# Kernel tuning notes

Hardware: AMD Instinct MI355X
Metric: run time of the kernel (lower is better)

Reference implementation:

```python
import jax, jax.numpy as jnp
import numpy as np

B, L, D, H = 4, 2048, 512, 512


def setup_inputs() -> dict:
    key = jax.random.key(0)
    ks = jax.random.split(key, 7)
    scale = D ** (-0.5)
    return {
        "x": jax.random.normal(ks[0], (B, L, D), jnp.float32),
        "hidden": jax.random.normal(ks[1], (B, D, H), jnp.float32),
        "log_base_lr": jnp.asarray(np.log(0.01), jnp.float32),
        "log_base_weight_decay": jnp.asarray(np.log(0.99), jnp.float32),
        "Wq": jax.random.normal(ks[2], (H, D), jnp.float32) * scale,
        "Wk": jax.random.normal(ks[3], (H, D), jnp.float32) * scale,
        "Wv": jax.random.normal(ks[4], (D, D), jnp.float32) * scale,
        "fc_lr_w": jax.random.normal(ks[5], (1, D), jnp.float32) * scale,
        "fc_lr_b": jnp.zeros((1,), jnp.float32),
        "fc_wd_w": jax.random.normal(ks[6], (1, D), jnp.float32) * scale,
        "fc_wd_b": jnp.zeros((1,), jnp.float32),
    }


def reference(x, hidden, log_base_lr, log_base_weight_decay, Wq, Wk, Wv,
              fc_lr_w, fc_lr_b, fc_wd_w, fc_wd_b):
    b, l, d = x.shape
    W_prev = hidden                                      # (b, d, h)
    query = jnp.einsum('bld,hd->blh', x, Wq)             # (b, l, h)
    key = jnp.einsum('bld,hd->blh', x, Wk)               # (b, l, h)
    value = jnp.einsum('bld,ed->ble', x, Wv)             # (b, l, d)

    lr = jnp.exp(log_base_lr) * jax.nn.sigmoid(
        jnp.einsum('bld,d->bl', x, fc_lr_w[0]) + fc_lr_b[0])        # (b, l)
    log_weight_decay = jnp.log(
        jnp.exp(log_base_weight_decay) * jax.nn.sigmoid(
            jnp.einsum('bld,d->bl', x, fc_wd_w[0]) + fc_wd_b[0]))   # (b, l)

    # cross-chunk decay: exp of prefix-sum of log decays
    wd_cross = jnp.exp(jnp.cumsum(log_weight_decay, axis=1))        # (b, l)

    # inner-chunk decay mask: (b, m, l), strictly-upper cumsum then upper triu
    rep = jnp.broadcast_to(log_weight_decay[:, None, :], (b, l, l))
    wd_inner = jnp.triu(jnp.exp(jnp.cumsum(jnp.triu(rep, 1), axis=2)))

    kq = jnp.einsum('blh,bmh->blm', key, query)          # (b, l, m)
    mask_kq = kq * wd_inner                              # (b, l, m)

    WpK_V = jnp.einsum('bdh,blh->bld', W_prev, key) - value         # (b, l, d)

    y_inner = -jnp.einsum('bld,bl,blm->bld', WpK_V, lr, mask_kq)
    y_cross = jnp.einsum('bdh,blh,bl->bld', W_prev, key, wd_cross)
    y = y_inner + y_cross

    W_next_inner = -jnp.einsum('bld,bl,blh->bdh', WpK_V, lr * wd_inner[:, :, -1], key)
    W_next_cross = W_prev * wd_cross[:, -1][:, None, None]
    W_next = W_next_inner + W_next_cross
    return (y, W_next)
```

## Files before the change

kernel.cpp:

```cpp
#include <hip/hip_runtime.h>
#include <cstdint>
#include <cstddef>

#define B_ 4
#define L_ 2048
#define D_ 512
#define H_ 512
#define CH 64
#define NC (L_ / CH)
#define NS 4

typedef unsigned short u16;
typedef __attribute__((ext_vector_type(8))) short short8v;
typedef __attribute__((ext_vector_type(4))) float f32x4;

typedef __attribute__((address_space(3))) unsigned lds_uint;
typedef const __attribute__((address_space(1))) unsigned glob_uint;

__device__ __forceinline__ void glds16(const u16* g, const u16* l) {
    __builtin_amdgcn_global_load_lds((glob_uint*)g, (lds_uint*)l, 16, 0, 0);
}

__device__ __forceinline__ u16 bf16_rne(float x) {
    union { float f; unsigned u; } v; v.f = x;
    unsigned r = v.u + 0x7fffu + ((v.u >> 16) & 1u);
    return (u16)(r >> 16);
}
__device__ __forceinline__ float bf16_tof(u16 h) {
    union { unsigned u; float f; } v; v.u = ((unsigned)h) << 16;
    return v.f;
}

__global__ __launch_bounds__(256) void k_prep(
    const float* __restrict__ x, const float* __restrict__ flr_w, const float* __restrict__ flr_b,
    const float* __restrict__ fwd_w, const float* __restrict__ fwd_b,
    const float* __restrict__ lblr, const float* __restrict__ lbwd,
    float* __restrict__ lr, float* __restrict__ lwd, float* __restrict__ wd,
    u16* __restrict__ xh)
{
    int bx = blockIdx.x;
    int wave = threadIdx.x >> 6;
    int lane = threadIdx.x & 63;
    int row  = bx * 4 + wave;
    const float4* xr = (const float4*)(x + (size_t)row * D_);
    const float4* wl = (const float4*)flr_w;
    const float4* ww = (const float4*)fwd_w;
    float zl = 0.f, zw = 0.f;
#pragma unroll
    for (int i = 0; i < 2; ++i) {
        int idx = lane + i * 64;
        float4 xv = xr[idx];
        float4 av = wl[idx];
        float4 bv = ww[idx];
        zl += xv.x*av.x + xv.y*av.y + xv.z*av.z + xv.w*av.w;
        zw += xv.x*bv.x + xv.y*bv.y + xv.z*bv.z + xv.w*bv.w;
        ushort4 h4;
        h4.x = bf16_rne(xv.x); h4.y = bf16_rne(xv.y);
        h4.z = bf16_rne(xv.z); h4.w = bf16_rne(xv.w);
        *(ushort4*)(xh + (size_t)row * D_ + idx * 4) = h4;
    }
#pragma unroll
    for (int off = 32; off; off >>= 1) {
        zl += __shfl_xor(zl, off, 64);
        zw += __shfl_xor(zw, off, 64);
    }
    if (lane == 0) {
        zl += flr_b[0];
        zw += fwd_b[0];
        float lrv = expf(lblr[0]) / (1.f + expf(-zl));
        float ls = (zw >= 0.f) ? (-log1pf(expf(-zw))) : (zw - log1pf(expf(zw)));
        float lw = lbwd[0] + ls;
        lr[row]  = lrv;
        lwd[row] = lw;
        wd[row]  = expf(lw);
    }
}

__global__ __launch_bounds__(256) void k_cumsum(
    const float* __restrict__ lwd, const float* __restrict__ lr,
    const float* __restrict__ Wq, const float* __restrict__ Wk, const float* __restrict__ Wv,
    const float* __restrict__ hid,
    u16* __restrict__ Wqh, u16* __restrict__ Wkh, u16* __restrict__ Wvh, u16* __restrict__ Wph,
    float* __restrict__ cum, float* __restrict__ wdc, float* __restrict__ c)
{
    int bx = blockIdx.x;
    if (bx >= B_) {
        int idx = bx - B_;
        int y = idx >> 8;
        const size_t DH = (size_t)D_ * H_;
        const float* s; u16* d;
        if      (y == 0) { s = Wq; d = Wqh; }
        else if (y == 1) { s = Wk; d = Wkh; }
        else if (y == 2) { s = Wv; d = Wvh; }
        else             { s = hid + (size_t)(y - 3) * DH; d = Wph + (size_t)(y - 3) * DH; }
        int i = ((idx & 255) * 256 + threadIdx.x) * 4;
        float4 v = *(const float4*)(s + i);
        ushort4 h4;
        h4.x = bf16_rne(v.x); h4.y = bf16_rne(v.y);
        h4.z = bf16_rne(v.z); h4.w = bf16_rne(v.w);
        *(ushort4*)(d + i) = h4;
        return;
    }
    int b = bx;
    int t = threadIdx.x;
    const float* in = lwd + (size_t)b * L_;
    float v[8];
    float s = 0.f;
#pragma unroll
    for (int j = 0; j < 8; ++j) { s += in[t*8 + j]; v[j] = s; }
    __shared__ float sd[256];
    __shared__ float totb;
    sd[t] = s;
    __syncthreads();
    for (int d = 1; d < 256; d <<= 1) {
        float xv = (t >= d) ? sd[t - d] : 0.f;
        __syncthreads();
        sd[t] += xv;
        __syncthreads();
    }
    float excl = sd[t] - s;
    if (t == 255) totb = sd[255];
    __syncthreads();
    float total = totb;
#pragma unroll
    for (int j = 0; j < 8; ++j) {
        int l = t*8 + j;
        float cv = excl + v[j];
        cum[(size_t)b*L_ + l] = cv;
        wdc[(size_t)b*L_ + l] = expf(cv);
        c[(size_t)b*L_ + l]   = lr[(size_t)b*L_ + l] * expf(total - cv);
    }
}


__device__ __forceinline__ void tile_src(int base_row, int ld, size_t& g0, size_t& g1) {
    int tid = threadIdx.x;
    int r = tid >> 2;
    int sw = ((tid & 3) ^ ((r >> 1) & 3)) * 8;
    g0 = (size_t)(base_row + r) * ld + sw;
    g1 = g0 + (size_t)64 * ld;
}
__device__ __forceinline__ int frag_off(int wbase, int f) {
    int lane = threadIdx.x & 63;
    int ra = wbase + f * 16 + (lane & 15);
    return ra * 64 + (((lane >> 4) ^ ((ra >> 1) & 3)) * 16);
}
__device__ __forceinline__ void mfma44(f32x4 acc[4][4], const short8v a[4], const short8v b[4]) {
#pragma unroll
    for (int i = 0; i < 4; ++i)
#pragma unroll
        for (int j = 0; j < 4; ++j)
            acc[i][j] = __builtin_amdgcn_mfma_f32_16x16x32_bf16(a[i], b[j], acc[i][j], 0, 0, 0);
}

__device__ __forceinline__ void core_dualB(
    char* smem, const u16* __restrict__ A_g,
    const u16* __restrict__ B0_g, const u16* __restrict__ B1_g,
    int lda, int ldb, int K, int m0, int n0, f32x4 acc0[4][4], f32x4 acc1[4][4])
{
    const int wv = threadIdx.x >> 6;
    const int wm = wv >> 1, wn = wv & 1;
    size_t aLo, aHi, bLo, bHi;
    tile_src(m0, lda, aLo, aHi);
    tile_src(n0, ldb, bLo, bHi);
    const int dLo = wv * 1024, dHi = 4096 + wv * 1024;
    int offA[4], offB[4];
#pragma unroll
    for (int f = 0; f < 4; ++f) { offA[f] = frag_off(wm * 64, f); offB[f] = frag_off(wn * 64, f); }
    auto stage = [&](int bi, int k0) {
        glds16(A_g  + aLo + k0, (const u16*)(smem + bi * 8192 + dLo));
        glds16(A_g  + aHi + k0, (const u16*)(smem + bi * 8192 + dHi));
        glds16(B0_g + bLo + k0, (const u16*)(smem + 24576 + bi * 8192 + dLo));
        glds16(B0_g + bHi + k0, (const u16*)(smem + 24576 + bi * 8192 + dHi));
        glds16(B1_g + bLo + k0, (const u16*)(smem + 49152 + bi * 8192 + dLo));
        glds16(B1_g + bHi + k0, (const u16*)(smem + 49152 + bi * 8192 + dHi));
    };
    const int nt = K >> 5;
    stage(0, 0);
    stage(1, 32);
    int bi = 0, bs = 2;
    for (int t = 0; t < nt; ++t) {
        if (t + 1 < nt) asm volatile("s_waitcnt vmcnt(6)" ::: "memory");
        else            asm volatile("s_waitcnt vmcnt(0)" ::: "memory");
        __builtin_amdgcn_s_barrier();
        asm volatile("" ::: "memory");
        if (t + 2 < nt) stage(bs, (t + 2) << 5);
        const char* bA  = smem + bi * 8192;
        const char* bB0 = smem + 24576 + bi * 8192;
        const char* bB1 = smem + 49152 + bi * 8192;
        short8v a[4], p[4], q[4];
#pragma unroll
        for (int f = 0; f < 4; ++f) {
            a[f] = *(const short8v*)(bA  + offA[f]);
            p[f] = *(const short8v*)(bB0 + offB[f]);
            q[f] = *(const short8v*)(bB1 + offB[f]);
        }
        __builtin_amdgcn_s_setprio(1);
        mfma44(acc0, a, p);
        mfma44(acc1, a, q);
        __builtin_amdgcn_s_setprio(0);
        asm volatile("" ::: "memory");
        bi = (bi == 2) ? 0 : bi + 1;
        bs = (bs == 2) ? 0 : bs + 1;
    }
    asm volatile("" ::: "memory");
    __builtin_amdgcn_s_barrier();
}

__device__ __forceinline__ void core_dualAB(
    char* smem, const u16* __restrict__ A0_g, const u16* __restrict__ A1_g,
    const u16* __restrict__ B0_g, const u16* __restrict__ B1_g,
    int lda, int ldb, int K, int m0, int n0, f32x4 acc0[4][4], f32x4 acc1[4][4])
{
    const int wv = threadIdx.x >> 6;
    const int wm = wv >> 1, wn = wv & 1;
    size_t aLo, aHi, bLo, bHi;
    tile_src(m0, lda, aLo, aHi);
    tile_src(n0, ldb, bLo, bHi);
    const int dLo = wv * 1024, dHi = 4096 + wv * 1024;
    int offA[4], offB[4];
#pragma unroll
    for (int f = 0; f < 4; ++f) { offA[f] = frag_off(wm * 64, f); offB[f] = frag_off(wn * 64, f); }
    auto stage = [&](int bi, int k0) {
        glds16(A0_g + aLo + k0, (const u16*)(smem + bi * 8192 + dLo));
        glds16(A0_g + aHi + k0, (const u16*)(smem + bi * 8192 + dHi));
        glds16(A1_g + aLo + k0, (const u16*)(smem + 24576 + bi * 8192 + dLo));
        glds16(A1_g + aHi + k0, (const u16*)(smem + 24576 + bi * 8192 + dHi));
        glds16(B0_g + bLo + k0, (const u16*)(smem + 49152 + bi * 8192 + dLo));
        glds16(B0_g + bHi + k0, (const u16*)(smem + 49152 + bi * 8192 + dHi));
        glds16(B1_g + bLo + k0, (const u16*)(smem + 73728 + bi * 8192 + dLo));
        glds16(B1_g + bHi + k0, (const u16*)(smem + 73728 + bi * 8192 + dHi));
    };
    const int nt = K >> 5;
    stage(0, 0);
    stage(1, 32);
    int bi = 0, bs = 2;
    for (int t = 0; t < nt; ++t) {
        if (t + 1 < nt) asm volatile("s_waitcnt vmcnt(8)" ::: "memory");
        else            asm volatile("s_waitcnt vmcnt(0)" ::: "memory");
        __builtin_amdgcn_s_barrier();
        asm volatile("" ::: "memory");
        if (t + 2 < nt) stage(bs, (t + 2) << 5);
        const char* bA0 = smem + bi * 8192;
        const char* bA1 = smem + 24576 + bi * 8192;
        const char* bB0 = smem + 49152 + bi * 8192;
        const char* bB1 = smem + 73728 + bi * 8192;
        short8v a[4], c[4], p[4], q[4];
#pragma unroll
        for (int f = 0; f < 4; ++f) {
            a[f] = *(const short8v*)(bA0 + offA[f]);
            c[f] = *(const short8v*)(bA1 + offA[f]);
            p[f] = *(const short8v*)(bB0 + offB[f]);
            q[f] = *(const short8v*)(bB1 + offB[f]);
        }
        __builtin_amdgcn_s_setprio(1);
        mfma44(acc0, a, p);
        mfma44(acc1, c, q);
        __builtin_amdgcn_s_setprio(0);
        asm volatile("" ::: "memory");
        bi = (bi == 2) ? 0 : bi + 1;
        bs = (bs == 2) ? 0 : bs + 1;
    }
    asm volatile("" ::: "memory");
    __builtin_amdgcn_s_barrier();
}

__device__ __forceinline__ void core_single(
    char* smem, const u16* __restrict__ A_g, const u16* __restrict__ B_g,
    int lda, int ldb, int K, int m0, int n0, f32x4 acc[4][4])
{
    const int wv = threadIdx.x >> 6;
    const int wm = wv >> 1, wn = wv & 1;
    size_t aLo, aHi, bLo, bHi;
    tile_src(m0, lda, aLo, aHi);
    tile_src(n0, ldb, bLo, bHi);
    const int dLo = wv * 1024, dHi = 4096 + wv * 1024;
    int offA[4], offB[4];
#pragma unroll
    for (int f = 0; f < 4; ++f) { offA[f] = frag_off(wm * 64, f); offB[f] = frag_off(wn * 64, f); }
    auto stage = [&](int bi, int k0) {
        glds16(A_g + aLo + k0, (const u16*)(smem + bi * 8192 + dLo));
        glds16(A_g + aHi + k0, (const u16*)(smem + bi * 8192 + dHi));
        glds16(B_g + bLo + k0, (const u16*)(smem + 24576 + bi * 8192 + dLo));
        glds16(B_g + bHi + k0, (const u16*)(smem + 24576 + bi * 8192 + dHi));
    };
    const int nt = K >> 5;
    stage(0, 0);
    stage(1, 32);
    int bi = 0, bs = 2;
    for (int t = 0; t < nt; ++t) {
        if (t + 1 < nt) asm volatile("s_waitcnt vmcnt(4)" ::: "memory");
        else            asm volatile("s_waitcnt vmcnt(0)" ::: "memory");
        __builtin_amdgcn_s_barrier();
        asm volatile("" ::: "memory");
        if (t + 2 < nt) stage(bs, (t + 2) << 5);
        const char* bA = smem + bi * 8192;
        const char* bB = smem + 24576 + bi * 8192;
        short8v a[4], p[4];
#pragma unroll
        for (int f = 0; f < 4; ++f) {
            a[f] = *(const short8v*)(bA + offA[f]);
            p[f] = *(const short8v*)(bB + offB[f]);
        }
        __builtin_amdgcn_s_setprio(1);
        mfma44(acc, a, p);
        __builtin_amdgcn_s_setprio(0);
        asm volatile("" ::: "memory");
        bi = (bi == 2) ? 0 : bi + 1;
        bs = (bs == 2) ? 0 : bs + 1;
    }
    asm volatile("" ::: "memory");
    __builtin_amdgcn_s_barrier();
}

__global__ __launch_bounds__(256, 1) void k_mfma_qk(
    const u16* __restrict__ xh,
    const u16* __restrict__ Wqh, const u16* __restrict__ Wkh,
    const float* __restrict__ cvec, const float* __restrict__ wd,
    u16* __restrict__ kh, u16* __restrict__ kcth, u16* __restrict__ Gloc)
{
    __shared__ __align__(16) char smem[73728];
    __shared__ float pwd[128];
    int flat = blockIdx.x;
    flat = (flat & 7) * 32 + (flat >> 3);
    int n0 = (flat & 3) * 128;
    int m0 = (flat >> 2) * 128;
    f32x4 accq[4][4], acck[4][4];
#pragma unroll
    for (int i = 0; i < 4; ++i)
#pragma unroll
    for (int j = 0; j < 4; ++j) { accq[i][j] = 0.f; acck[i][j] = 0.f; }
    core_dualB(smem, xh, Wqh, Wkh, D_, D_, D_, m0, n0, accq, acck);

    const int lane = threadIdx.x & 63;
    const int wv = threadIdx.x >> 6, wm = wv >> 1, wn = wv & 1;
    const int colq = lane & 15, rq = lane >> 4;

#pragma unroll
    for (int mf = 0; mf < 4; ++mf) {
        int grow0 = m0 + wm*64 + mf*16 + rq*4;
        float cv[4];
#pragma unroll
        for (int r = 0; r < 4; ++r) cv[r] = cvec[grow0 + r];
#pragma unroll
        for (int nf = 0; nf < 4; ++nf) {
            int gc = n0 + wn*64 + nf*16 + colq;
            f32x4 a = acck[mf][nf];
            ushort4 hc;
#pragma unroll
            for (int r = 0; r < 4; ++r) {
                kh[(size_t)(grow0 + r) * H_ + gc] = bf16_rne(a[r]);
                ((u16*)&hc)[r] = bf16_rne(cv[r] * a[r]);
            }
            int b = grow0 >> 11, lloc = grow0 & 2047;
            size_t tbase = (size_t)b * (H_ * L_) + (size_t)gc * L_ + lloc;
            *(ushort4*)(kcth + tbase) = hc;
        }
    }

    u16* g = (u16*)smem;
#pragma unroll
    for (int mf = 0; mf < 4; ++mf) {
        int rl0 = wm*64 + mf*16 + rq*4;
#pragma unroll
        for (int nf = 0; nf < 4; ++nf) {
            int cl = wn*64 + nf*16 + colq;
#pragma unroll
            for (int r = 0; r < 4; ++r)
                g[(rl0 + r)*128 + cl] = bf16_rne(accq[mf][nf][r]);
        }
    }
    if (threadIdx.x < 128) pwd[threadIdx.x] = wd[m0 + threadIdx.x];
    __syncthreads();
    {
        int col = threadIdx.x & 127;
        int base = (threadIdx.x >> 7) * 64;
        float G = bf16_tof(g[(base + 63)*128 + col]);
        for (int l = 62; l >= 0; --l) {
            float qv = bf16_tof(g[(base + l)*128 + col]);
            G = fmaf(pwd[base + l + 1], G, qv);
            g[(base + l)*128 + col] = bf16_rne(G);
        }
    }
    __syncthreads();
    int row = threadIdx.x >> 1, c0 = (threadIdx.x & 1) * 64;
    u16* dst = Gloc + (size_t)(m0 + row) * H_ + n0 + c0;
#pragma unroll
    for (int j = 0; j < 8; ++j)
        *(int4*)(dst + j*8) = *(const int4*)&g[row*128 + c0 + j*8];
}

__global__ __launch_bounds__(64) void k_scan_carry(
    const float* __restrict__ cum, const u16* __restrict__ Gloc, float* __restrict__ Gs)
{
    int b = blockIdx.x;
    int h = blockIdx.y * 64 + threadIdx.x;
    __shared__ float dec[NC];
    const float* cb = cum + (size_t)b * L_;
    if (threadIdx.x < NC - 1) dec[threadIdx.x] = expf(cb[(threadIdx.x + 1) * CH] - cb[threadIdx.x * CH]);
    __syncthreads();
    const u16* g = Gloc + (size_t)b * L_ * H_ + h;
    float* gs = Gs + (size_t)b * NC * H_ + h;
    float v[NC];
#pragma unroll
    for (int c = 0; c < NC; ++c)
        v[c] = bf16_tof(g[(size_t)(c * CH) * H_]);
    float G = v[NC - 1];
    gs[(size_t)(NC - 1) * H_] = G;
#pragma unroll
    for (int c = NC - 2; c >= 0; --c) {
        G = fmaf(dec[c], G, v[c]);
        gs[(size_t)c * H_] = G;
    }
}

__global__ __launch_bounds__(256) void k_sdot(
    const u16* __restrict__ kh,
    const u16* __restrict__ Gloc, const float* __restrict__ Gs,
    const float* __restrict__ cum, float* __restrict__ S)
{
    int wave = threadIdx.x >> 6, lane = threadIdx.x & 63;
    int row = blockIdx.x * 4 + wave;
    int b = row >> 11, l = row & 2047;
    int c = l / CH;
    float a = 0.f;
    const float* gsr = Gs;
    if (c < NC - 1) {
        a = expf(cum[((size_t)b << 11) + (size_t)((c + 1) * CH)] - cum[row]);
        gsr = Gs + ((size_t)(b * NC + c + 1)) * H_;
    }
    const u16* khr = kh + (size_t)row * H_;
    const u16* glr = Gloc + (size_t)row * H_;
    const float4* gq = (const float4*)gsr;
    float s = 0.f;
    int base = lane * 8;
    ushort4 h0 = *(const ushort4*)(khr + base);
    ushort4 h1 = *(const ushort4*)(khr + base + 4);
    ushort4 g0 = *(const ushort4*)(glr + base);
    ushort4 g1 = *(const ushort4*)(glr + base + 4);
    float4 s0 = gq[lane * 2];
    float4 s1 = gq[lane * 2 + 1];
    s += bf16_tof(h0.x) * fmaf(a, s0.x, bf16_tof(g0.x));
    s += bf16_tof(h0.y) * fmaf(a, s0.y, bf16_tof(g0.y));
    s += bf16_tof(h0.z) * fmaf(a, s0.z, bf16_tof(g0.z));
    s += bf16_tof(h0.w) * fmaf(a, s0.w, bf16_tof(g0.w));
    s += bf16_tof(h1.x) * fmaf(a, s1.x, bf16_tof(g1.x));
    s += bf16_tof(h1.y) * fmaf(a, s1.y, bf16_tof(g1.y));
    s += bf16_tof(h1.z) * fmaf(a, s1.z, bf16_tof(g1.z));
    s += bf16_tof(h1.w) * fmaf(a, s1.w, bf16_tof(g1.w));
#pragma unroll
    for (int off = 32; off; off >>= 1) s += __shfl_xor(s, off, 64);
    if (lane == 0) S[row] = s;
}

__global__ __launch_bounds__(256, 1) void k_mfma_ev(
    const u16* __restrict__ kh, const u16* __restrict__ xh,
    const u16* __restrict__ Wph, const u16* __restrict__ Wvh,
    const float* __restrict__ lr, const float* __restrict__ S, const float* __restrict__ wdc,
    float* __restrict__ y, u16* __restrict__ Eth)
{
    __shared__ __align__(16) char smem[98304];
    int flat = blockIdx.x;
    flat = (flat & 7) * 32 + (flat >> 3);
    int n0 = (flat & 3) * 128;
    int m0 = ((flat >> 2) & 15) * 128;
    int b  = flat >> 6;
    f32x4 acce[4][4], accv[4][4];
#pragma unroll
    for (int i = 0; i < 4; ++i)
#pragma unroll
    for (int j = 0; j < 4; ++j) { acce[i][j] = 0.f; accv[i][j] = 0.f; }
    core_dualAB(smem, kh + (size_t)b * L_ * H_, xh + (size_t)b * L_ * D_,
                Wph + (size_t)b * D_ * H_, Wvh,
                H_, H_, H_, m0, n0, acce, accv);

    const int lane = threadIdx.x & 63;
    const int wv = threadIdx.x >> 6, wm = wv >> 1, wn = wv & 1;
    const int colq = lane & 15, rq = lane >> 4;
#pragma unroll
    for (int mf = 0; mf < 4; ++mf) {
        int grow0 = m0 + wm*64 + mf*16 + rq*4;
        float ayv[4], wdv[4];
#pragma unroll
        for (int r = 0; r < 4; ++r) {
            size_t grow = (size_t)b * L_ + grow0 + r;
            ayv[r] = -lr[grow] * S[grow];
            wdv[r] = wdc[grow];
        }
#pragma unroll
        for (int nf = 0; nf < 4; ++nf) {
            int gc = n0 + wn*64 + nf*16 + colq;
            f32x4 ae = acce[mf][nf];
            f32x4 av = accv[mf][nf];
            ushort4 he;
#pragma unroll
            for (int r = 0; r < 4; ++r) {
                size_t gi = ((size_t)b * L_ + grow0 + r) * D_ + gc;
                float e = ae[r] - av[r];
                y[gi] = e * ayv[r] + ae[r] * wdv[r];
                ((u16*)&he)[r] = bf16_rne(e);
            }
            size_t tbase = (size_t)b * (D_ * L_) + (size_t)gc * L_ + grow0;
            *(ushort4*)(Eth + tbase) = he;
        }
    }
}

__global__ __launch_bounds__(256, 1) void k_mfma_wn(
    const u16* __restrict__ Eth, const u16* __restrict__ kcth,
    u16* __restrict__ wp)
{
    __shared__ __align__(16) char smem[49152];
    int flat = blockIdx.x;
    flat = (flat & 7) * 32 + (flat >> 3);
    int n0 = (flat & 3) * 128;
    int m0 = ((flat >> 2) & 3) * 128;
    int z  = flat >> 4;
    int b = z >> 2, s = z & 3;
    f32x4 acc[4][4];
#pragma unroll
    for (int i = 0; i < 4; ++i)
#pragma unroll
    for (int j = 0; j < 4; ++j) acc[i][j] = 0.f;
    const size_t pa = (size_t)b * (D_ * L_) + (size_t)s * (L_ / NS);
    const size_t pb = (size_t)b * (H_ * L_) + (size_t)s * (L_ / NS);
    core_single(smem, Eth + pa, kcth + pb, L_, L_, L_ / NS, m0, n0, acc);

    u16* out = wp + (size_t)z * D_ * H_;
    const int lane = threadIdx.x & 63;
    const int wv = threadIdx.x >> 6, wm = wv >> 1, wn = wv & 1;
    const int colq = lane & 15, rq = lane >> 4;
#pragma unroll
    for (int mf = 0; mf < 4; ++mf) {
        int grow0 = m0 + wm*64 + mf*16 + rq*4;
#pragma unroll
        for (int nf = 0; nf < 4; ++nf) {
            int gc = n0 + wn*64 + nf*16 + colq;
            f32x4 a = acc[mf][nf];
#pragma unroll
            for (int r = 0; r < 4; ++r) out[(size_t)(grow0 + r) * H_ + gc] = bf16_rne(a[r]);
        }
    }
}

__global__ __launch_bounds__(256) void k_wnext_reduce(
    const float* __restrict__ Wp, const u16* __restrict__ wp, const float* __restrict__ wdc,
    float* __restrict__ outw)
{
    size_t g = (size_t)blockIdx.x * 256 + threadIdx.x;
    size_t per = (size_t)D_ * H_ / 4;
    int b = (int)(g / per);
    size_t r = g % per;
    float wl = wdc[(size_t)b * L_ + (L_ - 1)];
    float4 w0 = ((const float4*)Wp)[g];
    float4 o;
    o.x = wl * w0.x; o.y = wl * w0.y; o.z = wl * w0.z; o.w = wl * w0.w;
#pragma unroll
    for (int s = 0; s < NS; ++s) {
        ushort4 p = ((const ushort4*)wp)[(size_t)(b * NS + s) * per + r];
        o.x -= bf16_tof(p.x); o.y -= bf16_tof(p.y);
        o.z -= bf16_tof(p.z); o.w -= bf16_tof(p.w);
    }
    ((float4*)outw)[g] = o;
}

extern "C" void kernel_launch(void* const* d_in, const int* in_sizes, int n_in,
                              void* d_out, int out_size, void* d_ws, size_t ws_size,
                              hipStream_t stream)
{
    (void)in_sizes; (void)n_in; (void)out_size; (void)ws_size;
    const float* x    = (const float*)d_in[0];
    const float* hid  = (const float*)d_in[1];
    const float* lblr = (const float*)d_in[2];
    const float* lbwd = (const float*)d_in[3];
    const float* Wq   = (const float*)d_in[4];
    const float* Wk   = (const float*)d_in[5];
    const float* Wv   = (const float*)d_in[6];
    const float* flrw = (const float*)d_in[7];
    const float* flrb = (const float*)d_in[8];
    const float* fwdw = (const float*)d_in[9];
    const float* fwdb = (const float*)d_in[10];
    float* out = (float*)d_out;

    const size_t BL  = (size_t)B_ * L_;
    const size_t BLH = BL * H_;
    const size_t DH  = (size_t)D_ * H_;

    char* w = (char*)d_ws;
    u16* Gloc_  = (u16*)w;   w += BLH * 2;
    u16* xh_    = (u16*)w;   w += BLH * 2;
    u16* kh_    = (u16*)w;   w += BLH * 2;
    u16* kcth_  = (u16*)w;   w += BLH * 2;
    u16* Eth_   = (u16*)w;   w += BLH * 2;
    u16* Wqh_   = (u16*)w;   w += DH * 2;
    u16* Wkh_   = (u16*)w;   w += DH * 2;
    u16* Wvh_   = (u16*)w;   w += DH * 2;
    u16* Wph_   = (u16*)w;   w += (size_t)B_ * DH * 2;
    float* lr_  = (float*)w; w += BL * 4;
    float* lwd_ = (float*)w; w += BL * 4;
    float* wd_  = (float*)w; w += BL * 4;
    float* cum_ = (float*)w; w += BL * 4;
    float* wdc_ = (float*)w; w += BL * 4;
    float* c_   = (float*)w; w += BL * 4;
    float* S_   = (float*)w; w += BL * 4;
    float* Gs_  = (float*)w; w += (size_t)B_ * NC * H_ * 4;

    u16* wp_ = Gloc_;

    k_prep<<<2048, 256, 0, stream>>>(x, flrw, flrb, fwdw, fwdb, lblr, lbwd,
                                     lr_, lwd_, wd_, xh_);
    k_cumsum<<<B_ + 7 * 256, 256, 0, stream>>>(lwd_, lr_, Wq, Wk, Wv, hid,
                                               Wqh_, Wkh_, Wvh_, Wph_,
                                               cum_, wdc_, c_);
    k_mfma_qk<<<256, 256, 0, stream>>>(xh_, Wqh_, Wkh_, c_, wd_,
                                       kh_, kcth_, Gloc_);
    k_scan_carry<<<dim3(B_, 8), 64, 0, stream>>>(cum_, Gloc_, Gs_);
    k_sdot<<<2048, 256, 0, stream>>>(kh_, Gloc_, Gs_, cum_, S_);
    k_mfma_ev<<<256, 256, 0, stream>>>(kh_, xh_, Wph_, Wvh_,
                                       lr_, S_, wdc_, out, Eth_);
    k_mfma_wn<<<256, 256, 0, stream>>>(Eth_, kcth_, wp_);
    k_wnext_reduce<<<1024, 256, 0, stream>>>(hid, wp_, wdc_, out + BLH);
}
```

Before: 82.05 us.

## Use 8-wave blocks with 2-stage LDS buffering in MFMA GEMM kernels

```diff
diff --git a/kernel.cpp b/kernel.cpp
--- a/kernel.cpp
+++ b/kernel.cpp
@@ -133,207 +133,197 @@
 }
 
 
-__device__ __forceinline__ void tile_src(int base_row, int ld, size_t& g0, size_t& g1) {
-    int tid = threadIdx.x;
+__device__ __forceinline__ void gg8(int lda, int ldb, int m0, int n0,
+                                    size_t& gA, size_t& gB, int& dst,
+                                    int offA[4], int offB[2]) {
+    const int tid = threadIdx.x;
+    const int lane = tid & 63;
+    const int wv = tid >> 6, wm = wv >> 2, wn = wv & 3;
     int r = tid >> 2;
     int sw = ((tid & 3) ^ ((r >> 1) & 3)) * 8;
-    g0 = (size_t)(base_row + r) * ld + sw;
-    g1 = g0 + (size_t)64 * ld;
-}
-__device__ __forceinline__ int frag_off(int wbase, int f) {
-    int lane = threadIdx.x & 63;
-    int ra = wbase + f * 16 + (lane & 15);
-    return ra * 64 + (((lane >> 4) ^ ((ra >> 1) & 3)) * 16);
-}
-__device__ __forceinline__ void mfma44(f32x4 acc[4][4], const short8v a[4], const short8v b[4]) {
-#pragma unroll
-    for (int i = 0; i < 4; ++i)
-#pragma unroll
-        for (int j = 0; j < 4; ++j)
-            acc[i][j] = __builtin_amdgcn_mfma_f32_16x16x32_bf16(a[i], b[j], acc[i][j], 0, 0, 0);
-}
-
-__device__ __forceinline__ void core_dualB(
+    gA = (size_t)(m0 + r) * lda + sw;
+    gB = (size_t)(n0 + r) * ldb + sw;
+    dst = wv * 1024;
+#pragma unroll
+    for (int f = 0; f < 4; ++f) {
+        int ra = wm * 64 + f * 16 + (lane & 15);
+        offA[f] = ra * 64 + (((lane >> 4) ^ ((ra >> 1) & 3)) * 16);
+    }
+#pragma unroll
+    for (int f = 0; f < 2; ++f) {
+        int rb = wn * 32 + f * 16 + (lane & 15);
+        offB[f] = rb * 64 + (((lane >> 4) ^ ((rb >> 1) & 3)) * 16);
+    }
+}
+
+__device__ __forceinline__ void core8_dualB(
     char* smem, const u16* __restrict__ A_g,
     const u16* __restrict__ B0_g, const u16* __restrict__ B1_g,
-    int lda, int ldb, int K, int m0, int n0, f32x4 acc0[4][4], f32x4 acc1[4][4])
-{
-    const int wv = threadIdx.x >> 6;
-    const int wm = wv >> 1, wn = wv & 1;
-    size_t aLo, aHi, bLo, bHi;
-    tile_src(m0, lda, aLo, aHi);
-    tile_src(n0, ldb, bLo, bHi);
-    const int dLo = wv * 1024, dHi = 4096 + wv * 1024;
-    int offA[4], offB[4];
-#pragma unroll
-    for (int f = 0; f < 4; ++f) { offA[f] = frag_off(wm * 64, f); offB[f] = frag_off(wn * 64, f); }
+    int lda, int ldb, int K, int m0, int n0, f32x4 acc0[4][2], f32x4 acc1[4][2])
+{
+    size_t gA, gB; int dst; int offA[4], offB[2];
+    gg8(lda, ldb, m0, n0, gA, gB, dst, offA, offB);
     auto stage = [&](int bi, int k0) {
-        glds16(A_g  + aLo + k0, (const u16*)(smem + bi * 8192 + dLo));
-        glds16(A_g  + aHi + k0, (const u16*)(smem + bi * 8192 + dHi));
-        glds16(B0_g + bLo + k0, (const u16*)(smem + 24576 + bi * 8192 + dLo));
-        glds16(B0_g + bHi + k0, (const u16*)(smem + 24576 + bi * 8192 + dHi));
-        glds16(B1_g + bLo + k0, (const u16*)(smem + 49152 + bi * 8192 + dLo));
-        glds16(B1_g + bHi + k0, (const u16*)(smem + 49152 + bi * 8192 + dHi));
+        glds16(A_g  + gA + k0, (const u16*)(smem + bi * 8192 + dst));
+        glds16(B0_g + gB + k0, (const u16*)(smem + 16384 + bi * 8192 + dst));
+        glds16(B1_g + gB + k0, (const u16*)(smem + 32768 + bi * 8192 + dst));
     };
     const int nt = K >> 5;
     stage(0, 0);
-    stage(1, 32);
-    int bi = 0, bs = 2;
+    if (nt > 1) stage(1, 32);
     for (int t = 0; t < nt; ++t) {
-        if (t + 1 < nt) asm volatile("s_waitcnt vmcnt(6)" ::: "memory");
+        const int bi = t & 1;
+        if (t + 1 < nt) asm volatile("s_waitcnt vmcnt(3)" ::: "memory");
         else            asm volatile("s_waitcnt vmcnt(0)" ::: "memory");
         __builtin_amdgcn_s_barrier();
         asm volatile("" ::: "memory");
-        if (t + 2 < nt) stage(bs, (t + 2) << 5);
         const char* bA  = smem + bi * 8192;
-        const char* bB0 = smem + 24576 + bi * 8192;
-        const char* bB1 = smem + 49152 + bi * 8192;
-        short8v a[4], p[4], q[4];
-#pragma unroll
-        for (int f = 0; f < 4; ++f) {
-            a[f] = *(const short8v*)(bA  + offA[f]);
+        const char* bB0 = smem + 16384 + bi * 8192;
+        const char* bB1 = smem + 32768 + bi * 8192;
+        short8v a[4], p[2], q[2];
+#pragma unroll
+        for (int f = 0; f < 4; ++f) a[f] = *(const short8v*)(bA + offA[f]);
+#pragma unroll
+        for (int f = 0; f < 2; ++f) {
             p[f] = *(const short8v*)(bB0 + offB[f]);
             q[f] = *(const short8v*)(bB1 + offB[f]);
         }
         __builtin_amdgcn_s_setprio(1);
-        mfma44(acc0, a, p);
-        mfma44(acc1, a, q);
+#pragma unroll
+        for (int i = 0; i < 4; ++i)
+#pragma unroll
+            for (int j = 0; j < 2; ++j)
+                acc0[i][j] = __builtin_amdgcn_mfma_f32_16x16x32_bf16(a[i], p[j], acc0[i][j], 0, 0, 0);
+#pragma unroll
+        for (int i = 0; i < 4; ++i)
+#pragma unroll
+            for (int j = 0; j < 2; ++j)
+                acc1[i][j] = __builtin_amdgcn_mfma_f32_16x16x32_bf16(a[i], q[j], acc1[i][j], 0, 0, 0);
         __builtin_amdgcn_s_setprio(0);
         asm volatile("" ::: "memory");
-        bi = (bi == 2) ? 0 : bi + 1;
-        bs = (bs == 2) ? 0 : bs + 1;
-    }
-    asm volatile("" ::: "memory");
-    __builtin_amdgcn_s_barrier();
-}
-
-__device__ __forceinline__ void core_dualAB(
+        __builtin_amdgcn_s_barrier();
+        asm volatile("" ::: "memory");
+        if (t + 2 < nt) stage(bi, (t + 2) << 5);
+    }
+}
+
+__device__ __forceinline__ void core8_dualAB(
     char* smem, const u16* __restrict__ A0_g, const u16* __restrict__ A1_g,
     const u16* __restrict__ B0_g, const u16* __restrict__ B1_g,
-    int lda, int ldb, int K, int m0, int n0, f32x4 acc0[4][4], f32x4 acc1[4][4])
-{
-    const int wv = threadIdx.x >> 6;
-    const int wm = wv >> 1, wn = wv & 1;
-    size_t aLo, aHi, bLo, bHi;
-    tile_src(m0, lda, aLo, aHi);
-    tile_src(n0, ldb, bLo, bHi);
-    const int dLo = wv * 1024, dHi = 4096 + wv * 1024;
-    int offA[4], offB[4];
-#pragma unroll
-    for (int f = 0; f < 4; ++f) { offA[f] = frag_off(wm * 64, f); offB[f] = frag_off(wn * 64, f); }
+    int lda, int ldb, int K, int m0, int n0, f32x4 acc0[4][2], f32x4 acc1[4][2])
+{
+    size_t gA, gB; int dst; int offA[4], offB[2];
+    gg8(lda, ldb, m0, n0, gA, gB, dst, offA, offB);
     auto stage = [&](int bi, int k0) {
-        glds16(A0_g + aLo + k0, (const u16*)(smem + bi * 8192 + dLo));
-        glds16(A0_g + aHi + k0, (const u16*)(smem + bi * 8192 + dHi));
-        glds16(A1_g + aLo + k0, (const u16*)(smem + 24576 + bi * 8192 + dLo));
-        glds16(A1_g + aHi + k0, (const u16*)(smem + 24576 + bi * 8192 + dHi));
-        glds16(B0_g + bLo + k0, (const u16*)(smem + 49152 + bi * 8192 + dLo));
-        glds16(B0_g + bHi + k0, (const u16*)(smem + 49152 + bi * 8192 + dHi));
-        glds16(B1_g + bLo + k0, (const u16*)(smem + 73728 + bi * 8192 + dLo));
-        glds16(B1_g + bHi + k0, (const u16*)(smem + 73728 + bi * 8192 + dHi));
+        glds16(A0_g + gA + k0, (const u16*)(smem + bi * 8192 + dst));
+        glds16(A1_g + gA + k0, (const u16*)(smem + 16384 + bi * 8192 + dst));
+        glds16(B0_g + gB + k0, (const u16*)(smem + 32768 + bi * 8192 + dst));
+        glds16(B1_g + gB + k0, (const u16*)(smem + 49152 + bi * 8192 + dst));
     };
     const int nt = K >> 5;
     stage(0, 0);
-    stage(1, 32);
-    int bi = 0, bs = 2;
+    if (nt > 1) stage(1, 32);
     for (int t = 0; t < nt; ++t) {
-        if (t + 1 < nt) asm volatile("s_waitcnt vmcnt(8)" ::: "memory");
+        const int bi = t & 1;
+        if (t + 1 < nt) asm volatile("s_waitcnt vmcnt(4)" ::: "memory");
         else            asm volatile("s_waitcnt vmcnt(0)" ::: "memory");
         __builtin_amdgcn_s_barrier();
         asm volatile("" ::: "memory");
-        if (t + 2 < nt) stage(bs, (t + 2) << 5);
         const char* bA0 = smem + bi * 8192;
-        const char* bA1 = smem + 24576 + bi * 8192;
-        const char* bB0 = smem + 49152 + bi * 8192;
-        const char* bB1 = smem + 73728 + bi * 8192;
-        short8v a[4], c[4], p[4], q[4];
+        const char* bA1 = smem + 16384 + bi * 8192;
+        const char* bB0 = smem + 32768 + bi * 8192;
+        const char* bB1 = smem + 49152 + bi * 8192;
+        short8v a[4], c[4], p[2], q[2];
 #pragma unroll
         for (int f = 0; f < 4; ++f) {
             a[f] = *(const short8v*)(bA0 + offA[f]);
             c[f] = *(const short8v*)(bA1 + offA[f]);
+        }
+#pragma unroll
+        for (int f = 0; f < 2; ++f) {
             p[f] = *(const short8v*)(bB0 + offB[f]);
             q[f] = *(const short8v*)(bB1 + offB[f]);
         }
         __builtin_amdgcn_s_setprio(1);
-        mfma44(acc0, a, p);
-        mfma44(acc1, c, q);
+#pragma unroll
+        for (int i = 0; i < 4; ++i)
+#pragma unroll
+            for (int j = 0; j < 2; ++j)
+                acc0[i][j] = __builtin_amdgcn_mfma_f32_16x16x32_bf16(a[i], p[j], acc0[i][j], 0, 0, 0);
+#pragma unroll
+        for (int i = 0; i < 4; ++i)
+#pragma unroll
+            for (int j = 0; j < 2; ++j)
+                acc1[i][j] = __builtin_amdgcn_mfma_f32_16x16x32_bf16(c[i], q[j], acc1[i][j], 0, 0, 0);
         __builtin_amdgcn_s_setprio(0);
         asm volatile("" ::: "memory");
-        bi = (bi == 2) ? 0 : bi + 1;
-        bs = (bs == 2) ? 0 : bs + 1;
-    }
-    asm volatile("" ::: "memory");
-    __builtin_amdgcn_s_barrier();
-}
-
-__device__ __forceinline__ void core_single(
+        __builtin_amdgcn_s_barrier();
+        asm volatile("" ::: "memory");
+        if (t + 2 < nt) stage(bi, (t + 2) << 5);
+    }
+}
+
+__device__ __forceinline__ void core8_single(
     char* smem, const u16* __restrict__ A_g, const u16* __restrict__ B_g,
-    int lda, int ldb, int K, int m0, int n0, f32x4 acc[4][4])
-{
-    const int wv = threadIdx.x >> 6;
-    const int wm = wv >> 1, wn = wv & 1;
-    size_t aLo, aHi, bLo, bHi;
-    tile_src(m0, lda, aLo, aHi);
-    tile_src(n0, ldb, bLo, bHi);
-    const int dLo = wv * 1024, dHi = 4096 + wv * 1024;
-    int offA[4], offB[4];
-#pragma unroll
-    for (int f = 0; f < 4; ++f) { offA[f] = frag_off(wm * 64, f); offB[f] = frag_off(wn * 64, f); }
+    int lda, int ldb, int K, int m0, int n0, f32x4 acc[4][2])
+{
+    size_t gA, gB; int dst; int offA[4], offB[2];
+    gg8(lda, ldb, m0, n0, gA, gB, dst, offA, offB);
     auto stage = [&](int bi, int k0) {
-        glds16(A_g + aLo + k0, (const u16*)(smem + bi * 8192 + dLo));
-        glds16(A_g + aHi + k0, (const u16*)(smem + bi * 8192 + dHi));
-        glds16(B_g + bLo + k0, (const u16*)(smem + 24576 + bi * 8192 + dLo));
-        glds16(B_g + bHi + k0, (const u16*)(smem + 24576 + bi * 8192 + dHi));
+        glds16(A_g + gA + k0, (const u16*)(smem + bi * 8192 + dst));
+        glds16(B_g + gB + k0, (const u16*)(smem + 16384 + bi * 8192 + dst));
     };
     const int nt = K >> 5;
     stage(0, 0);
-    stage(1, 32);
-    int bi = 0, bs = 2;
+    if (nt > 1) stage(1, 32);
     for (int t = 0; t < nt; ++t) {
-        if (t + 1 < nt) asm volatile("s_waitcnt vmcnt(4)" ::: "memory");
+        const int bi = t & 1;
+        if (t + 1 < nt) asm volatile("s_waitcnt vmcnt(2)" ::: "memory");
         else            asm volatile("s_waitcnt vmcnt(0)" ::: "memory");
         __builtin_amdgcn_s_barrier();
         asm volatile("" ::: "memory");
-        if (t + 2 < nt) stage(bs, (t + 2) << 5);
         const char* bA = smem + bi * 8192;
-        const char* bB = smem + 24576 + bi * 8192;
-        short8v a[4], p[4];
-#pragma unroll
-        for (int f = 0; f < 4; ++f) {
-            a[f] = *(const short8v*)(bA + offA[f]);
-            p[f] = *(const short8v*)(bB + offB[f]);
-        }
+        const char* bB = smem + 16384 + bi * 8192;
+        short8v a[4], p[2];
+#pragma unroll
+        for (int f = 0; f < 4; ++f) a[f] = *(const short8v*)(bA + offA[f]);
+#pragma unroll
+        for (int f = 0; f < 2; ++f) p[f] = *(const short8v*)(bB + offB[f]);
         __builtin_amdgcn_s_setprio(1);
-        mfma44(acc, a, p);
+#pragma unroll
+        for (int i = 0; i < 4; ++i)
+#pragma unroll
+            for (int j = 0; j < 2; ++j)
+                acc[i][j] = __builtin_amdgcn_mfma_f32_16x16x32_bf16(a[i], p[j], acc[i][j], 0, 0, 0);
         __builtin_amdgcn_s_setprio(0);
         asm volatile("" ::: "memory");
-        bi = (bi == 2) ? 0 : bi + 1;
-        bs = (bs == 2) ? 0 : bs + 1;
-    }
-    asm volatile("" ::: "memory");
-    __builtin_amdgcn_s_barrier();
-}
-
-__global__ __launch_bounds__(256, 1) void k_mfma_qk(
+        __builtin_amdgcn_s_barrier();
+        asm volatile("" ::: "memory");
+        if (t + 2 < nt) stage(bi, (t + 2) << 5);
+    }
+}
+
+__global__ __launch_bounds__(512) void k_mfma_qk(
     const u16* __restrict__ xh,
     const u16* __restrict__ Wqh, const u16* __restrict__ Wkh,
     const float* __restrict__ cvec, const float* __restrict__ wd,
     u16* __restrict__ kh, u16* __restrict__ kcth, u16* __restrict__ Gloc)
 {
-    __shared__ __align__(16) char smem[73728];
+    __shared__ __align__(16) char smem[49152];
     __shared__ float pwd[128];
     int flat = blockIdx.x;
     flat = (flat & 7) * 32 + (flat >> 3);
     int n0 = (flat & 3) * 128;
     int m0 = (flat >> 2) * 128;
-    f32x4 accq[4][4], acck[4][4];
+    f32x4 accq[4][2], acck[4][2];
 #pragma unroll
     for (int i = 0; i < 4; ++i)
 #pragma unroll
-    for (int j = 0; j < 4; ++j) { accq[i][j] = 0.f; acck[i][j] = 0.f; }
-    core_dualB(smem, xh, Wqh, Wkh, D_, D_, D_, m0, n0, accq, acck);
+    for (int j = 0; j < 2; ++j) { accq[i][j] = 0.f; acck[i][j] = 0.f; }
+    core8_dualB(smem, xh, Wqh, Wkh, D_, D_, D_, m0, n0, accq, acck);
 
     const int lane = threadIdx.x & 63;
-    const int wv = threadIdx.x >> 6, wm = wv >> 1, wn = wv & 1;
+    const int wv = threadIdx.x >> 6, wm = wv >> 2, wn = wv & 3;
     const int colq = lane & 15, rq = lane >> 4;
 
 #pragma unroll
@@ -343,8 +333,8 @@
 #pragma unroll
         for (int r = 0; r < 4; ++r) cv[r] = cvec[grow0 + r];
 #pragma unroll
-        for (int nf = 0; nf < 4; ++nf) {
-            int gc = n0 + wn*64 + nf*16 + colq;
+        for (int nf = 0; nf < 2; ++nf) {
+            int gc = n0 + wn*32 + nf*16 + colq;
             f32x4 a = acck[mf][nf];
             ushort4 hc;
 #pragma unroll
@@ -363,8 +353,8 @@
     for (int mf = 0; mf < 4; ++mf) {
         int rl0 = wm*64 + mf*16 + rq*4;
 #pragma unroll
-        for (int nf = 0; nf < 4; ++nf) {
-            int cl = wn*64 + nf*16 + colq;
+        for (int nf = 0; nf < 2; ++nf) {
+            int cl = wn*32 + nf*16 + colq;
 #pragma unroll
             for (int r = 0; r < 4; ++r)
                 g[(rl0 + r)*128 + cl] = bf16_rne(accq[mf][nf][r]);
@@ -372,8 +362,8 @@
     }
     if (threadIdx.x < 128) pwd[threadIdx.x] = wd[m0 + threadIdx.x];
     __syncthreads();
-    {
-        int col = threadIdx.x & 127;
+    if (threadIdx.x < 256) {
+        int col  = threadIdx.x & 127;
         int base = (threadIdx.x >> 7) * 64;
         float G = bf16_tof(g[(base + 63)*128 + col]);
         for (int l = 62; l >= 0; --l) {
@@ -383,10 +373,10 @@
         }
     }
     __syncthreads();
-    int row = threadIdx.x >> 1, c0 = (threadIdx.x & 1) * 64;
+    int row = threadIdx.x >> 2, c0 = (threadIdx.x & 3) * 32;
     u16* dst = Gloc + (size_t)(m0 + row) * H_ + n0 + c0;
 #pragma unroll
-    for (int j = 0; j < 8; ++j)
+    for (int j = 0; j < 4; ++j)
         *(int4*)(dst + j*8) = *(const int4*)&g[row*128 + c0 + j*8];
 }
 
@@ -453,29 +443,29 @@
     if (lane == 0) S[row] = s;
 }
 
-__global__ __launch_bounds__(256, 1) void k_mfma_ev(
+__global__ __launch_bounds__(512) void k_mfma_ev(
     const u16* __restrict__ kh, const u16* __restrict__ xh,
     const u16* __restrict__ Wph, const u16* __restrict__ Wvh,
     const float* __restrict__ lr, const float* __restrict__ S, const float* __restrict__ wdc,
     float* __restrict__ y, u16* __restrict__ Eth)
 {
-    __shared__ __align__(16) char smem[98304];
+    __shared__ __align__(16) char smem[65536];
     int flat = blockIdx.x;
     flat = (flat & 7) * 32 + (flat >> 3);
     int n0 = (flat & 3) * 128;
     int m0 = ((flat >> 2) & 15) * 128;
     int b  = flat >> 6;
-    f32x4 acce[4][4], accv[4][4];
+    f32x4 acce[4][2], accv[4][2];
 #pragma unroll
     for (int i = 0; i < 4; ++i)
 #pragma unroll
-    for (int j = 0; j < 4; ++j) { acce[i][j] = 0.f; accv[i][j] = 0.f; }
-    core_dualAB(smem, kh + (size_t)b * L_ * H_, xh + (size_t)b * L_ * D_,
-                Wph + (size_t)b * D_ * H_, Wvh,
-                H_, H_, H_, m0, n0, acce, accv);
+    for (int j = 0; j < 2; ++j) { acce[i][j] = 0.f; accv[i][j] = 0.f; }
+    core8_dualAB(smem, kh + (size_t)b * L_ * H_, xh + (size_t)b * L_ * D_,
+                 Wph + (size_t)b * D_ * H_, Wvh,
+                 H_, H_, H_, m0, n0, acce, accv);
 
     const int lane = threadIdx.x & 63;
-    const int wv = threadIdx.x >> 6, wm = wv >> 1, wn = wv & 1;
+    const int wv = threadIdx.x >> 6, wm = wv >> 2, wn = wv & 3;
     const int colq = lane & 15, rq = lane >> 4;
 #pragma unroll
     for (int mf = 0; mf < 4; ++mf) {
@@ -488,8 +478,8 @@
             wdv[r] = wdc[grow];
         }
 #pragma unroll
-        for (int nf = 0; nf < 4; ++nf) {
-            int gc = n0 + wn*64 + nf*16 + colq;
+        for (int nf = 0; nf < 2; ++nf) {
+            int gc = n0 + wn*32 + nf*16 + colq;
             f32x4 ae = acce[mf][nf];
             f32x4 av = accv[mf][nf];
             ushort4 he;
@@ -506,36 +496,36 @@
     }
 }
 
-__global__ __launch_bounds__(256, 1) void k_mfma_wn(
+__global__ __launch_bounds__(512) void k_mfma_wn(
     const u16* __restrict__ Eth, const u16* __restrict__ kcth,
     u16* __restrict__ wp)
 {
-    __shared__ __align__(16) char smem[49152];
+    __shared__ __align__(16) char smem[32768];
     int flat = blockIdx.x;
     flat = (flat & 7) * 32 + (flat >> 3);
     int n0 = (flat & 3) * 128;
     int m0 = ((flat >> 2) & 3) * 128;
     int z  = flat >> 4;
     int b = z >> 2, s = z & 3;
-    f32x4 acc[4][4];
+    f32x4 acc[4][2];
 #pragma unroll
     for (int i = 0; i < 4; ++i)
 #pragma unroll
-    for (int j = 0; j < 4; ++j) acc[i][j] = 0.f;
+    for (int j = 0; j < 2; ++j) acc[i][j] = 0.f;
     const size_t pa = (size_t)b * (D_ * L_) + (size_t)s * (L_ / NS);
     const size_t pb = (size_t)b * (H_ * L_) + (size_t)s * (L_ / NS);
-    core_single(smem, Eth + pa, kcth + pb, L_, L_, L_ / NS, m0, n0, acc);
+    core8_single(smem, Eth + pa, kcth + pb, L_, L_, L_ / NS, m0, n0, acc);
 
     u16* out = wp + (size_t)z * D_ * H_;
     const int lane = threadIdx.x & 63;
-    const int wv = threadIdx.x >> 6, wm = wv >> 1, wn = wv & 1;
+    const int wv = threadIdx.x >> 6, wm = wv >> 2, wn = wv & 3;
     const int colq = lane & 15, rq = lane >> 4;
 #pragma unroll
     for (int mf = 0; mf < 4; ++mf) {
         int grow0 = m0 + wm*64 + mf*16 + rq*4;
 #pragma unroll
-        for (int nf = 0; nf < 4; ++nf) {
-            int gc = n0 + wn*64 + nf*16 + colq;
+        for (int nf = 0; nf < 2; ++nf) {
+            int gc = n0 + wn*32 + nf*16 + colq;
             f32x4 a = acc[mf][nf];
 #pragma unroll
             for (int r = 0; r < 4; ++r) out[(size_t)(grow0 + r) * H_ + gc] = bf16_rne(a[r]);
@@ -612,12 +602,12 @@
     k_cumsum<<<B_ + 7 * 256, 256, 0, stream>>>(lwd_, lr_, Wq, Wk, Wv, hid,
                                                Wqh_, Wkh_, Wvh_, Wph_,
                                                cum_, wdc_, c_);
-    k_mfma_qk<<<256, 256, 0, stream>>>(xh_, Wqh_, Wkh_, c_, wd_,
+    k_mfma_qk<<<256, 512, 0, stream>>>(xh_, Wqh_, Wkh_, c_, wd_,
                                        kh_, kcth_, Gloc_);
     k_scan_carry<<<dim3(B_, 8), 64, 0, stream>>>(cum_, Gloc_, Gs_);
     k_sdot<<<2048, 256, 0, stream>>>(kh_, Gloc_, Gs_, cum_, S_);
-    k_mfma_ev<<<256, 256, 0, stream>>>(kh_, xh_, Wph_, Wvh_,
+    k_mfma_ev<<<256, 512, 0, stream>>>(kh_, xh_, Wph_, Wvh_,
                                        lr_, S_, wdc_, out, Eth_);
-    k_mfma_wn<<<256, 256, 0, stream>>>(Eth_, kcth_, wp_);
+    k_mfma_wn<<<256, 512, 0, stream>>>(Eth_, kcth_, wp_);
     k_wnext_reduce<<<1024, 256, 0, stream>>>(hid, wp_, wdc_, out + BLH);
 }
```

Result: faster. 75.53 us (-7.9%).
